# Kernel tuning notes

Measured on AMD Instinct MI355X. Metric: run time of the kernel, lower is better.

The kernel has to match this reference:

```python
import jax, jax.numpy as jnp
import numpy as np

N = 50000
C = 128
E = 800000
STEPS = 3


def setup_inputs() -> dict:
    key = jax.random.key(0)
    ks = jax.random.split(key, 8)
    x = jax.random.normal(ks[0], (N, C), dtype=jnp.float32)
    edge_index = jax.random.randint(ks[1], (2, E), 0, N, dtype=jnp.int64)
    s = 1.0 / np.sqrt(C)
    W_lin = jax.random.uniform(ks[2], (C, C), jnp.float32, -s, s)   # nn.Linear(C, C, bias=False)
    W_ih = jax.random.uniform(ks[3], (3 * C, C), jnp.float32, -s, s)  # GRUCell weight_ih
    W_hh = jax.random.uniform(ks[4], (3 * C, C), jnp.float32, -s, s)  # GRUCell weight_hh
    b_ih = jax.random.uniform(ks[5], (3 * C,), jnp.float32, -s, s)
    b_hh = jax.random.uniform(ks[6], (3 * C,), jnp.float32, -s, s)
    return {"x": x, "edge_index": edge_index, "W_lin": W_lin,
            "W_ih": W_ih, "W_hh": W_hh, "b_ih": b_ih, "b_hh": b_hh}


def _gru_cell(inp, h, W_ih, W_hh, b_ih, b_hh):
    # torch.nn.GRUCell math
    gi = inp @ W_ih.T + b_ih   # [N, 3C]
    gh = h @ W_hh.T + b_hh     # [N, 3C]
    i_r, i_z, i_n = jnp.split(gi, 3, axis=-1)
    h_r, h_z, h_n = jnp.split(gh, 3, axis=-1)
    r = jax.nn.sigmoid(i_r + h_r)
    z = jax.nn.sigmoid(i_z + h_z)
    n = jnp.tanh(i_n + r * h_n)
    return (1.0 - z) * n + z * h


def reference(x, edge_index, W_lin, W_ih, W_hh, b_ih, b_hh):
    src = edge_index[0]
    dst = edge_index[1]
    state = x
    for _ in range(STEPS):
        m = state @ W_lin.T                       # [N, C] dense transform
        msgs = jnp.take(m, src, axis=0)           # [E, C] gather
        propagated = jax.ops.segment_sum(msgs, dst, num_segments=N)  # scatter-add
        state = _gru_cell(propagated, state, W_ih, W_hh, b_ih, b_hh)
    return state
```

## Files before the change

kernel.cpp:

```cpp
#include <hip/hip_runtime.h>

#define NN 50000
#define CC 128
#define EE 800000
#define NT 1563
#define NBLK 196

typedef short bf16x8 __attribute__((ext_vector_type(8)));
typedef float f32x4 __attribute__((ext_vector_type(4)));

__device__ __forceinline__ float bf2f(unsigned int u16) {
  union { unsigned int u; float f; } x; x.u = u16 << 16; return x.f;
}
__device__ __forceinline__ unsigned short f2bf(float f) {
  union { float f; unsigned int u; } x; x.f = f;
  unsigned int u = x.u;
  unsigned int r = (u + 0x7fffu + ((u >> 16) & 1u)) >> 16;
  return (unsigned short)r;
}
__device__ __forceinline__ float fsigmoid(float x) {
  return __fdividef(1.f, 1.f + __expf(-x));
}
__device__ __forceinline__ float ftanh(float x) {
  return 1.f - __fdividef(2.f, 1.f + __expf(2.f * x));
}

__global__ void cast_f2b_k(const float* __restrict__ in, unsigned short* __restrict__ out, int n4) {
  int i = blockIdx.x * blockDim.x + threadIdx.x;
  int stride = gridDim.x * blockDim.x;
  for (; i < n4; i += stride) {
    float4 v = ((const float4*)in)[i];
    ushort4 o;
    o.x = f2bf(v.x); o.y = f2bf(v.y); o.z = f2bf(v.z); o.w = f2bf(v.w);
    ((ushort4*)out)[i] = o;
  }
}

__global__ __launch_bounds__(256) void wprep_k(const float* __restrict__ Wih,
                                               const float* __restrict__ Wlin,
                                               const float* __restrict__ Whh,
                                               unsigned short* __restrict__ Wcb,
                                               unsigned short* __restrict__ Whhb) {
  if (blockIdx.x < 192) {
    int gid = blockIdx.x * 256 + threadIdx.x;
    int i = gid >> 7, j = gid & 127;
    float acc = 0.f;
    #pragma unroll 8
    for (int k = 0; k < 128; ++k)
      acc += Wih[i * 128 + k] * Wlin[k * 128 + j];
    Wcb[i * 128 + j] = f2bf(acc);
  } else {
    int i = (blockIdx.x - 192) * 256 + threadIdx.x;
    float4 v = ((const float4*)Whh)[i];
    ushort4 o;
    o.x = f2bf(v.x); o.y = f2bf(v.y); o.z = f2bf(v.z); o.w = f2bf(v.w);
    ((ushort4*)Whhb)[i] = o;
  }
}

__global__ void zero_k(int* __restrict__ p, int n) {
  int i = blockIdx.x * blockDim.x + threadIdx.x;
  if (i < n) p[i] = 0;
}

__global__ void hist_k(const int* __restrict__ dst, int* __restrict__ cnt,
                       int* __restrict__ rank, int n) {
  int i = blockIdx.x * blockDim.x + threadIdx.x;
  if (i < n) rank[i] = atomicAdd(&cnt[dst[i]], 1);
}

__global__ __launch_bounds__(256) void scan1_k(const int* __restrict__ cnt,
                                               int* __restrict__ rowptr,
                                               int* __restrict__ bsum, int N) {
  __shared__ int wtot[4];
  int tid = threadIdx.x, lane = tid & 63, w = tid >> 6;
  int i = blockIdx.x * 256 + tid;
  int v = (i < N) ? cnt[i] : 0;
  int x = v;
  #pragma unroll
  for (int off = 1; off < 64; off <<= 1) {
    int t = __shfl_up(x, off, 64);
    if (lane >= off) x += t;
  }
  if (lane == 63) wtot[w] = x;
  __syncthreads();
  int woff = 0;
  for (int j = 0; j < w; ++j) woff += wtot[j];
  int excl = x - v + woff;
  if (i < N) rowptr[i] = excl;
  if (tid == 255) bsum[blockIdx.x] = excl + v;
}

__global__ __launch_bounds__(256) void scan2_k(int* __restrict__ bsum, int* __restrict__ rowptr, int NB) {
  __shared__ int wtot[4];
  int tid = threadIdx.x, lane = tid & 63, w = tid >> 6;
  int v = (tid < NB) ? bsum[tid] : 0;
  int x = v;
  #pragma unroll
  for (int off = 1; off < 64; off <<= 1) {
    int t = __shfl_up(x, off, 64);
    if (lane >= off) x += t;
  }
  if (lane == 63) wtot[w] = x;
  __syncthreads();
  int woff = 0;
  for (int j = 0; j < w; ++j) woff += wtot[j];
  int excl = x - v + woff;
  if (tid < NB) bsum[tid] = excl;
  if (tid == 255) rowptr[NN] = excl + v;
}

__global__ void scan3_k(int* __restrict__ rowptr, const int* __restrict__ bsum, int N) {
  int i = blockIdx.x * 256 + threadIdx.x;
  if (i < N) rowptr[i] = rowptr[i] + bsum[i >> 8];
}

__global__ void fill_k(const int* __restrict__ src, const int* __restrict__ dst,
                       const int* __restrict__ rank, const int* __restrict__ rowptr,
                       int* __restrict__ colx, int n4) {
  int i = blockIdx.x * blockDim.x + threadIdx.x;
  if (i < n4) {
    int4 s = ((const int4*)src)[i];
    int4 d = ((const int4*)dst)[i];
    int4 r = ((const int4*)rank)[i];
    colx[rowptr[d.x] + r.x] = s.x;
    colx[rowptr[d.y] + r.y] = s.y;
    colx[rowptr[d.z] + r.z] = s.z;
    colx[rowptr[d.w] + r.w] = s.w;
  }
}

__global__ __launch_bounds__(256) void agg2_k(const unsigned short* __restrict__ M,
                                              const int* __restrict__ rowptr,
                                              const int* __restrict__ colx,
                                              unsigned short* __restrict__ P, int N) {
  int wid = (blockIdx.x * 256 + threadIdx.x) >> 6;
  int lane = threadIdx.x & 63;
  if (wid >= N) return;
  int beg = rowptr[wid], end = rowptr[wid + 1];
  int half = lane >> 5, li = lane & 31;
  float a0 = 0.f, a1 = 0.f, a2 = 0.f, a3 = 0.f;
  int n = end - beg;
  int i = 0;
  for (; i + 8 <= n; i += 8) {
    int e = beg + i + half;
    int s0 = colx[e], s1 = colx[e + 2], s2 = colx[e + 4], s3 = colx[e + 6];
    uint2 v0 = *(const uint2*)(M + s0 * CC + li * 4);
    uint2 v1 = *(const uint2*)(M + s1 * CC + li * 4);
    uint2 v2 = *(const uint2*)(M + s2 * CC + li * 4);
    uint2 v3 = *(const uint2*)(M + s3 * CC + li * 4);
    a0 += bf2f(v0.x & 0xffffu); a1 += bf2f(v0.x >> 16); a2 += bf2f(v0.y & 0xffffu); a3 += bf2f(v0.y >> 16);
    a0 += bf2f(v1.x & 0xffffu); a1 += bf2f(v1.x >> 16); a2 += bf2f(v1.y & 0xffffu); a3 += bf2f(v1.y >> 16);
    a0 += bf2f(v2.x & 0xffffu); a1 += bf2f(v2.x >> 16); a2 += bf2f(v2.y & 0xffffu); a3 += bf2f(v2.y >> 16);
    a0 += bf2f(v3.x & 0xffffu); a1 += bf2f(v3.x >> 16); a2 += bf2f(v3.y & 0xffffu); a3 += bf2f(v3.y >> 16);
  }
  for (; i + 2 <= n; i += 2) {
    int e = beg + i + half;
    int s = colx[e];
    uint2 v = *(const uint2*)(M + s * CC + li * 4);
    a0 += bf2f(v.x & 0xffffu); a1 += bf2f(v.x >> 16); a2 += bf2f(v.y & 0xffffu); a3 += bf2f(v.y >> 16);
  }
  if (i < n && half == 0) {
    int s = colx[beg + i];
    uint2 v = *(const uint2*)(M + s * CC + li * 4);
    a0 += bf2f(v.x & 0xffffu); a1 += bf2f(v.x >> 16); a2 += bf2f(v.y & 0xffffu); a3 += bf2f(v.y >> 16);
  }
  a0 += __shfl_xor(a0, 32, 64);
  a1 += __shfl_xor(a1, 32, 64);
  a2 += __shfl_xor(a2, 32, 64);
  a3 += __shfl_xor(a3, 32, 64);
  if (half == 0) {
    uint2 o;
    o.x = (unsigned int)f2bf(a0) | ((unsigned int)f2bf(a1) << 16);
    o.y = (unsigned int)f2bf(a2) | ((unsigned int)f2bf(a3) << 16);
    *(uint2*)(P + wid * CC + li * 4) = o;
  }
}

__global__ __launch_bounds__(512, 2) void gru4_k(const unsigned short* __restrict__ Pb,
                                                 const unsigned short* __restrict__ Sb_in,
                                                 unsigned short* __restrict__ Sb_out,
                                                 float* __restrict__ fout,
                                                 const unsigned short* __restrict__ Wcb,
                                                 const unsigned short* __restrict__ Whhb,
                                                 const float* __restrict__ bih,
                                                 const float* __restrict__ bhh) {
  __shared__ unsigned short sA[2][2][32][128];
  const int tid = threadIdx.x;
  const int lane = tid & 63, w = tid >> 6;
  const int l15 = lane & 15, l4 = lane >> 4;

  const int cg = w * 16 + l15;

  bf16x8 Breg[6][4];
  #pragma unroll
  for (int pi = 0; pi < 6; ++pi) {
    const unsigned short* Wm = (pi < 3) ? Wcb : Whhb;
    int p = (pi < 3) ? pi : pi - 3;
    const unsigned short* base = Wm + (p * 128 + cg) * 128 + l4 * 8;
    #pragma unroll
    for (int ks = 0; ks < 4; ++ks)
      Breg[pi][ks] = *(const bf16x8*)(base + ks * 32);
  }

  const float bir = bih[cg], biz = bih[cg + 128], bin_ = bih[cg + 256];
  const float bhr = bhh[cg], bhz = bhh[cg + 128], bhn = bhh[cg + 256];

  auto loadA = [&](int t, uint4* r) {
    int rowbase = t * 32;
    #pragma unroll
    for (int k = 0; k < 2; ++k) {
      int idx = k * 512 + tid;
      int mat = idx >> 9, j = idx & 511, row = j >> 4, ch = j & 15;
      int grow = rowbase + row;
      const unsigned short* srcp = mat ? Sb_in : Pb;
      r[k] = (grow < NN) ? *(const uint4*)(srcp + grow * 128 + ch * 8) : make_uint4(0, 0, 0, 0);
    }
  };
  auto writeA = [&](int buf, const uint4* r) {
    #pragma unroll
    for (int k = 0; k < 2; ++k) {
      int idx = k * 512 + tid;
      int mat = idx >> 9, j = idx & 511, row = j >> 4, ch = j & 15;
      *(uint4*)&sA[buf][mat][row][((ch ^ (row & 15)) * 8)] = r[k];
    }
  };

  uint4 pre[2];
  int t0 = blockIdx.x;
  loadA(t0, pre);
  writeA(0, pre);
  int cur = 0;
  for (int t = t0; t < NT; t += 256) {
    __syncthreads();
    int tn = t + 256;
    uint4 nxt[2];
    if (tn < NT) loadA(tn, nxt);

    f32x4 acc[6][2] = {};
    #pragma unroll
    for (int ks = 0; ks < 4; ++ks) {
      bf16x8 a[2][2];
      #pragma unroll
      for (int mat = 0; mat < 2; ++mat)
        #pragma unroll
        for (int rt = 0; rt < 2; ++rt) {
          int row = rt * 16 + l15;
          a[mat][rt] = *(const bf16x8*)&sA[cur][mat][row][(((ks * 4 + l4) ^ l15) * 8)];
        }
      #pragma unroll
      for (int pi = 0; pi < 6; ++pi) {
        int am = (pi < 3) ? 0 : 1;
        acc[pi][0] = __builtin_amdgcn_mfma_f32_16x16x32_bf16(a[am][0], Breg[pi][ks], acc[pi][0], 0, 0, 0);
        acc[pi][1] = __builtin_amdgcn_mfma_f32_16x16x32_bf16(a[am][1], Breg[pi][ks], acc[pi][1], 0, 0, 0);
      }
    }

    int rowbase = t * 32;
    #pragma unroll
    for (int rt = 0; rt < 2; ++rt)
      #pragma unroll
      for (int i = 0; i < 4; ++i) {
        int row_loc = rt * 16 + l4 * 4 + i;
        int row = rowbase + row_loc;
        if (row < NN) {
          float gir = acc[0][rt][i] + bir;
          float giz = acc[1][rt][i] + biz;
          float gin = acc[2][rt][i] + bin_;
          float ghr = acc[3][rt][i] + bhr;
          float ghz = acc[4][rt][i] + bhz;
          float ghn = acc[5][rt][i] + bhn;
          float r = fsigmoid(gir + ghr);
          float z = fsigmoid(giz + ghz);
          float n = ftanh(gin + r * ghn);
          float h = bf2f((unsigned int)sA[cur][1][row_loc][(((cg >> 3) ^ (row_loc & 15)) << 3) + (cg & 7)]);
          float o = n + z * (h - n);
          if (fout) fout[row * 128 + cg] = o;
          else      Sb_out[row * 128 + cg] = f2bf(o);
        }
      }
    if (tn < NT) writeA(cur ^ 1, nxt);
    cur ^= 1;
  }
}

extern "C" void kernel_launch(void* const* d_in, const int* in_sizes, int n_in,
                              void* d_out, int out_size, void* d_ws, size_t ws_size,
                              hipStream_t stream) {
  const float* x    = (const float*)d_in[0];
  const int*   ei   = (const int*)d_in[1];
  const float* Wlin = (const float*)d_in[2];
  const float* Wih  = (const float*)d_in[3];
  const float* Whh  = (const float*)d_in[4];
  const float* bih  = (const float*)d_in[5];
  const float* bhh  = (const float*)d_in[6];
  float* out = (float*)d_out;

  char* ws = (char*)d_ws;
  size_t off = 0;
  auto alloc = [&](size_t bytes) -> void* {
    void* p = ws + off;
    off += (bytes + 255) & ~(size_t)255;
    return p;
  };
  unsigned short* SbA  = (unsigned short*)alloc((size_t)NN * CC * 2);
  unsigned short* SbB  = (unsigned short*)alloc((size_t)NN * CC * 2);
  unsigned short* Prb  = (unsigned short*)alloc((size_t)NN * CC * 2);
  unsigned short* Wcb  = (unsigned short*)alloc((size_t)3 * CC * CC * 2);
  unsigned short* Whhb = (unsigned short*)alloc((size_t)3 * CC * CC * 2);
  int* rowptr = (int*)alloc((size_t)(NN + 1) * 4);
  int* cnt    = (int*)alloc((size_t)NN * 4);
  int* rank   = (int*)alloc((size_t)EE * 4);
  int* colx   = (int*)alloc((size_t)EE * 4);
  int* bsum   = (int*)alloc(256 * 4);

  const int* srcI = ei;
  const int* dstI = ei + EE;

  cast_f2b_k<<<1024, 256, 0, stream>>>(x, SbA, NN * CC / 4);
  wprep_k<<<240, 256, 0, stream>>>(Wih, Wlin, Whh, Wcb, Whhb);

  zero_k<<<NBLK, 256, 0, stream>>>(cnt, NN);
  hist_k<<<EE / 256, 256, 0, stream>>>(dstI, cnt, rank, EE);
  scan1_k<<<NBLK, 256, 0, stream>>>(cnt, rowptr, bsum, NN);
  scan2_k<<<1, 256, 0, stream>>>(bsum, rowptr, NBLK);
  scan3_k<<<NBLK, 256, 0, stream>>>(rowptr, bsum, NN);
  fill_k<<<(EE / 4 + 255) / 256, 256, 0, stream>>>(srcI, dstI, rank, rowptr, colx, EE / 4);

  const int aggBlocks = (NN + 3) / 4;

  agg2_k<<<aggBlocks, 256, 0, stream>>>(SbA, rowptr, colx, Prb, NN);
  gru4_k<<<256, 512, 0, stream>>>(Prb, SbA, SbB, nullptr, Wcb, Whhb, bih, bhh);
  agg2_k<<<aggBlocks, 256, 0, stream>>>(SbB, rowptr, colx, Prb, NN);
  gru4_k<<<256, 512, 0, stream>>>(Prb, SbB, SbA, nullptr, Wcb, Whhb, bih, bhh);
  agg2_k<<<aggBlocks, 256, 0, stream>>>(SbA, rowptr, colx, Prb, NN);
  gru4_k<<<256, 512, 0, stream>>>(Prb, SbA, SbB, out, Wcb, Whhb, bih, bhh);
}
```

Baseline: 336.0 us.

## Replicate histogram counters and widen aggregation gathers to 16-byte loads

The edge histogram now uses eight replicated count arrays, selected by block index, to spread atomic contention. The scan folds these into per-replica offsets that the fill kernel uses when placing edges. The aggregation kernel switches from two 32-lane halves with 8-byte loads to four 16-lane slots with 16-byte loads, so each wave processes four edges per step. The cost is a larger counter array to zero and scan, plus more accumulator registers in the aggregation kernel.

```diff
diff --git a/kernel.cpp b/kernel.cpp
--- a/kernel.cpp
+++ b/kernel.cpp
@@ -63,19 +63,30 @@
   if (i < n) p[i] = 0;
 }
 
-__global__ void hist_k(const int* __restrict__ dst, int* __restrict__ cnt,
+__global__ void hist_k(const int* __restrict__ dst, int* __restrict__ cntrep,
                        int* __restrict__ rank, int n) {
   int i = blockIdx.x * blockDim.x + threadIdx.x;
-  if (i < n) rank[i] = atomicAdd(&cnt[dst[i]], 1);
-}
-
-__global__ __launch_bounds__(256) void scan1_k(const int* __restrict__ cnt,
+  int rep = blockIdx.x & 7;
+  if (i < n) rank[i] = atomicAdd(&cntrep[rep * NN + dst[i]], 1);
+}
+
+__global__ __launch_bounds__(256) void scan1_k(int* __restrict__ cntrep,
                                                int* __restrict__ rowptr,
                                                int* __restrict__ bsum, int N) {
   __shared__ int wtot[4];
   int tid = threadIdx.x, lane = tid & 63, w = tid >> 6;
   int i = blockIdx.x * 256 + tid;
-  int v = (i < N) ? cnt[i] : 0;
+  int v = 0;
+  if (i < N) {
+    int s = 0;
+    #pragma unroll
+    for (int r = 0; r < 8; ++r) {
+      int c = cntrep[r * NN + i];
+      cntrep[r * NN + i] = s;
+      s += c;
+    }
+    v = s;
+  }
   int x = v;
   #pragma unroll
   for (int off = 1; off < 64; off <<= 1) {
@@ -117,20 +128,21 @@
 
 __global__ void fill_k(const int* __restrict__ src, const int* __restrict__ dst,
                        const int* __restrict__ rank, const int* __restrict__ rowptr,
-                       int* __restrict__ colx, int n4) {
+                       const int* __restrict__ cntrep, int* __restrict__ colx, int n4) {
   int i = blockIdx.x * blockDim.x + threadIdx.x;
   if (i < n4) {
     int4 s = ((const int4*)src)[i];
     int4 d = ((const int4*)dst)[i];
     int4 r = ((const int4*)rank)[i];
-    colx[rowptr[d.x] + r.x] = s.x;
-    colx[rowptr[d.y] + r.y] = s.y;
-    colx[rowptr[d.z] + r.z] = s.z;
-    colx[rowptr[d.w] + r.w] = s.w;
-  }
-}
-
-__global__ __launch_bounds__(256) void agg2_k(const unsigned short* __restrict__ M,
+    int base = ((i >> 6) & 7) * NN;
+    colx[rowptr[d.x] + cntrep[base + d.x] + r.x] = s.x;
+    colx[rowptr[d.y] + cntrep[base + d.y] + r.y] = s.y;
+    colx[rowptr[d.z] + cntrep[base + d.z] + r.z] = s.z;
+    colx[rowptr[d.w] + cntrep[base + d.w] + r.w] = s.w;
+  }
+}
+
+__global__ __launch_bounds__(256) void agg3_k(const unsigned short* __restrict__ M,
                                               const int* __restrict__ rowptr,
                                               const int* __restrict__ colx,
                                               unsigned short* __restrict__ P, int N) {
@@ -138,42 +150,52 @@
   int lane = threadIdx.x & 63;
   if (wid >= N) return;
   int beg = rowptr[wid], end = rowptr[wid + 1];
-  int half = lane >> 5, li = lane & 31;
-  float a0 = 0.f, a1 = 0.f, a2 = 0.f, a3 = 0.f;
+  int slot = lane >> 4, li = lane & 15;
+  float a0 = 0.f, a1 = 0.f, a2 = 0.f, a3 = 0.f, a4 = 0.f, a5 = 0.f, a6 = 0.f, a7 = 0.f;
+  #define ACC(v) do { \
+    a0 += bf2f((v).x & 0xffffu); a1 += bf2f((v).x >> 16); \
+    a2 += bf2f((v).y & 0xffffu); a3 += bf2f((v).y >> 16); \
+    a4 += bf2f((v).z & 0xffffu); a5 += bf2f((v).z >> 16); \
+    a6 += bf2f((v).w & 0xffffu); a7 += bf2f((v).w >> 16); } while (0)
   int n = end - beg;
   int i = 0;
-  for (; i + 8 <= n; i += 8) {
-    int e = beg + i + half;
-    int s0 = colx[e], s1 = colx[e + 2], s2 = colx[e + 4], s3 = colx[e + 6];
-    uint2 v0 = *(const uint2*)(M + s0 * CC + li * 4);
-    uint2 v1 = *(const uint2*)(M + s1 * CC + li * 4);
-    uint2 v2 = *(const uint2*)(M + s2 * CC + li * 4);
-    uint2 v3 = *(const uint2*)(M + s3 * CC + li * 4);
-    a0 += bf2f(v0.x & 0xffffu); a1 += bf2f(v0.x >> 16); a2 += bf2f(v0.y & 0xffffu); a3 += bf2f(v0.y >> 16);
-    a0 += bf2f(v1.x & 0xffffu); a1 += bf2f(v1.x >> 16); a2 += bf2f(v1.y & 0xffffu); a3 += bf2f(v1.y >> 16);
-    a0 += bf2f(v2.x & 0xffffu); a1 += bf2f(v2.x >> 16); a2 += bf2f(v2.y & 0xffffu); a3 += bf2f(v2.y >> 16);
-    a0 += bf2f(v3.x & 0xffffu); a1 += bf2f(v3.x >> 16); a2 += bf2f(v3.y & 0xffffu); a3 += bf2f(v3.y >> 16);
-  }
-  for (; i + 2 <= n; i += 2) {
-    int e = beg + i + half;
+  for (; i + 16 <= n; i += 16) {
+    int e = beg + i + slot;
+    int s0 = colx[e], s1 = colx[e + 4], s2 = colx[e + 8], s3 = colx[e + 12];
+    uint4 v0 = *(const uint4*)(M + s0 * CC + li * 8);
+    uint4 v1 = *(const uint4*)(M + s1 * CC + li * 8);
+    uint4 v2 = *(const uint4*)(M + s2 * CC + li * 8);
+    uint4 v3 = *(const uint4*)(M + s3 * CC + li * 8);
+    ACC(v0); ACC(v1); ACC(v2); ACC(v3);
+  }
+  for (; i + 4 <= n; i += 4) {
+    int e = beg + i + slot;
     int s = colx[e];
-    uint2 v = *(const uint2*)(M + s * CC + li * 4);
-    a0 += bf2f(v.x & 0xffffu); a1 += bf2f(v.x >> 16); a2 += bf2f(v.y & 0xffffu); a3 += bf2f(v.y >> 16);
-  }
-  if (i < n && half == 0) {
-    int s = colx[beg + i];
-    uint2 v = *(const uint2*)(M + s * CC + li * 4);
-    a0 += bf2f(v.x & 0xffffu); a1 += bf2f(v.x >> 16); a2 += bf2f(v.y & 0xffffu); a3 += bf2f(v.y >> 16);
-  }
-  a0 += __shfl_xor(a0, 32, 64);
-  a1 += __shfl_xor(a1, 32, 64);
-  a2 += __shfl_xor(a2, 32, 64);
-  a3 += __shfl_xor(a3, 32, 64);
-  if (half == 0) {
-    uint2 o;
+    uint4 v = *(const uint4*)(M + s * CC + li * 8);
+    ACC(v);
+  }
+  int rem = n - i;
+  if (slot < rem) {
+    int e = beg + i + slot;
+    int s = colx[e];
+    uint4 v = *(const uint4*)(M + s * CC + li * 8);
+    ACC(v);
+  }
+  #undef ACC
+  #pragma unroll
+  for (int m = 16; m <= 32; m <<= 1) {
+    a0 += __shfl_xor(a0, m, 64); a1 += __shfl_xor(a1, m, 64);
+    a2 += __shfl_xor(a2, m, 64); a3 += __shfl_xor(a3, m, 64);
+    a4 += __shfl_xor(a4, m, 64); a5 += __shfl_xor(a5, m, 64);
+    a6 += __shfl_xor(a6, m, 64); a7 += __shfl_xor(a7, m, 64);
+  }
+  if (slot == 0) {
+    uint4 o;
     o.x = (unsigned int)f2bf(a0) | ((unsigned int)f2bf(a1) << 16);
     o.y = (unsigned int)f2bf(a2) | ((unsigned int)f2bf(a3) << 16);
-    *(uint2*)(P + wid * CC + li * 4) = o;
+    o.z = (unsigned int)f2bf(a4) | ((unsigned int)f2bf(a5) << 16);
+    o.w = (unsigned int)f2bf(a6) | ((unsigned int)f2bf(a7) << 16);
+    *(uint4*)(P + wid * CC + li * 8) = o;
   }
 }
 
@@ -309,7 +331,7 @@
   unsigned short* Wcb  = (unsigned short*)alloc((size_t)3 * CC * CC * 2);
   unsigned short* Whhb = (unsigned short*)alloc((size_t)3 * CC * CC * 2);
   int* rowptr = (int*)alloc((size_t)(NN + 1) * 4);
-  int* cnt    = (int*)alloc((size_t)NN * 4);
+  int* cntrep = (int*)alloc((size_t)8 * NN * 4);
   int* rank   = (int*)alloc((size_t)EE * 4);
   int* colx   = (int*)alloc((size_t)EE * 4);
   int* bsum   = (int*)alloc(256 * 4);
@@ -320,19 +342,19 @@
   cast_f2b_k<<<1024, 256, 0, stream>>>(x, SbA, NN * CC / 4);
   wprep_k<<<240, 256, 0, stream>>>(Wih, Wlin, Whh, Wcb, Whhb);
 
-  zero_k<<<NBLK, 256, 0, stream>>>(cnt, NN);
-  hist_k<<<EE / 256, 256, 0, stream>>>(dstI, cnt, rank, EE);
-  scan1_k<<<NBLK, 256, 0, stream>>>(cnt, rowptr, bsum, NN);
+  zero_k<<<(8 * NN + 255) / 256, 256, 0, stream>>>(cntrep, 8 * NN);
+  hist_k<<<EE / 256, 256, 0, stream>>>(dstI, cntrep, rank, EE);
+  scan1_k<<<NBLK, 256, 0, stream>>>(cntrep, rowptr, bsum, NN);
   scan2_k<<<1, 256, 0, stream>>>(bsum, rowptr, NBLK);
   scan3_k<<<NBLK, 256, 0, stream>>>(rowptr, bsum, NN);
-  fill_k<<<(EE / 4 + 255) / 256, 256, 0, stream>>>(srcI, dstI, rank, rowptr, colx, EE / 4);
+  fill_k<<<(EE / 4 + 255) / 256, 256, 0, stream>>>(srcI, dstI, rank, rowptr, cntrep, colx, EE / 4);
 
   const int aggBlocks = (NN + 3) / 4;
 
-  agg2_k<<<aggBlocks, 256, 0, stream>>>(SbA, rowptr, colx, Prb, NN);
+  agg3_k<<<aggBlocks, 256, 0, stream>>>(SbA, rowptr, colx, Prb, NN);
   gru4_k<<<256, 512, 0, stream>>>(Prb, SbA, SbB, nullptr, Wcb, Whhb, bih, bhh);
-  agg2_k<<<aggBlocks, 256, 0, stream>>>(SbB, rowptr, colx, Prb, NN);
+  agg3_k<<<aggBlocks, 256, 0, stream>>>(SbB, rowptr, colx, Prb, NN);
   gru4_k<<<256, 512, 0, stream>>>(Prb, SbB, SbA, nullptr, Wcb, Whhb, bih, bhh);
-  agg2_k<<<aggBlocks, 256, 0, stream>>>(SbA, rowptr, colx, Prb, NN);
+  agg3_k<<<aggBlocks, 256, 0, stream>>>(SbA, rowptr, colx, Prb, NN);
   gru4_k<<<256, 512, 0, stream>>>(Prb, SbA, SbB, out, Wcb, Whhb, bih, bhh);
 }
```

Measured after the change: 329.4 us. 2.0% less time.
